# Optimization experiments

Hardware: AMD Instinct MI355X
Metric: run time of the kernel (lower is better)

Reference implementation:

```python
import jax, jax.numpy as jnp
import numpy as np

H = 16
DK = 64
N_PERSIS = 512
D_MODEL = 1024


def setup_inputs() -> dict:
    key = jax.random.key(0)
    ks = jax.random.split(key, 9)
    bs, n, d = 4, 4096, D_MODEL
    inp = {
        "Q": jax.random.normal(ks[0], (bs, n, d), jnp.float32),
        "K": jax.random.normal(ks[1], (bs, n, d), jnp.float32),
        "V": jax.random.normal(ks[2], (bs, n, d), jnp.float32),
        # nn.Linear(d, d, bias=False) weights, applied as x @ W.T
        "WQ": jax.random.normal(ks[3], (d, d), jnp.float32) / np.sqrt(d),
        "WK": jax.random.normal(ks[4], (d, d), jnp.float32) / np.sqrt(d),
        "WV": jax.random.normal(ks[5], (d, d), jnp.float32) / np.sqrt(d),
        "WO": jax.random.normal(ks[6], (d, d), jnp.float32) / np.sqrt(d),
        # persistent memory: MK ~ N(0, 1/dk) * dk**0.5 ; MV ~ N(0, 1/n_persis) * n_persis**0.5
        "MK": jax.random.normal(ks[7], (1, H, N_PERSIS, DK), jnp.float32) * (DK ** 0.5 / DK),
        "MV": jax.random.normal(ks[8], (1, H, N_PERSIS, DK), jnp.float32) * (N_PERSIS ** 0.5 / N_PERSIS),
    }
    return inp


def _split_heads(x, h, dk):
    bs, n, _ = x.shape
    return x.reshape(bs, n, h, dk).transpose(0, 2, 1, 3)  # bs,h,n,dk


def reference(Q, K, V, WQ, WK, WV, WO, MK, MV):
    bs, n, d = Q.shape
    h, dk = MK.shape[1], MK.shape[3]
    q = _split_heads(Q @ WQ.T, h, dk)
    k = _split_heads(K @ WK.T, h, dk)
    v = _split_heads(V @ WV.T, h, dk)
    # concat persistent memory tokens along sequence dim -> m = n + n_persis
    k = jnp.concatenate([k, jnp.broadcast_to(MK, (bs,) + MK.shape[1:])], axis=2)
    v = jnp.concatenate([v, jnp.broadcast_to(MV, (bs,) + MV.shape[1:])], axis=2)
    # dual-softmax linear attention (GDN)
    lamb = jax.nn.softmax(k * dk ** 0.25, axis=2)   # softmax over sequence (m)
    beta = jax.nn.softmax(q, axis=-1)               # softmax over features (dk)
    kv = jnp.einsum('bhmd,bhme->bhde', lamb, v)     # small dk x dk summary
    z = jnp.einsum('bhnd,bhde->bhne', beta, kv)     # bs,h,n,dk
    y = z.transpose(0, 2, 1, 3).reshape(bs, n, h * dk)
    return y @ WO.T
```

## Files before the change

### kernel.cpp

```cpp
#include <hip/hip_runtime.h>
#include <stdint.h>

typedef __attribute__((ext_vector_type(8))) short short8;
typedef __attribute__((ext_vector_type(4))) short short4v;
typedef __attribute__((ext_vector_type(4))) float float4v;
typedef __attribute__((ext_vector_type(4))) unsigned int uint4v;

#define NSEQ   4096
#define DMODEL 1024
#define NHEAD  16
#define DK     64
#define NP     512
#define MTOT   4608
#define NCH    24
#define CH     192
#define SCALE  2.8284271247461903f

__device__ __forceinline__ float b2f(unsigned short u) {
  union { unsigned u; float f; } x; x.u = ((unsigned)u) << 16; return x.f;
}
__device__ __forceinline__ unsigned short f2b(float f) {
  union { float f; unsigned u; } x; x.f = f;
  unsigned r = x.u + 0x7fffu + ((x.u >> 16) & 1u);
  return (unsigned short)(r >> 16);
}
__device__ __forceinline__ void split1(float x, unsigned short& h, unsigned short& l) {
  h = f2b(x);
  l = f2b(x - b2f(h));
}
__device__ __forceinline__ void gload16(const void* g, void* l) {
  __builtin_amdgcn_global_load_lds((const __attribute__((address_space(1))) void*)g,
                                   (__attribute__((address_space(3))) void*)l,
                                   16, 0, 0);
}
__device__ __forceinline__ short8 ld8(const unsigned* p) {
  union { short8 s; short4v h[2]; } u;
  u.h[0] = *(const short4v*)p;
  u.h[1] = *(const short4v*)(p + 2);
  return u.s;
}

__device__ __forceinline__ void swz(int lin, long& brow, long& bcol) {
  brow = (long)(((lin & 7) << 4) | (lin >> 6)) * 128;
  bcol = (long)((lin >> 3) & 7) * 128;
}

__global__ __launch_bounds__(256) void cvt_split(const float* __restrict__ s,
                                                 unsigned short* __restrict__ hi,
                                                 unsigned short* __restrict__ lo, int n) {
  const int i = (blockIdx.x * 256 + threadIdx.x) * 8;
  if (i + 8 > n) return;
  float4v x0 = *(const float4v*)(s + i);
  float4v x1 = *(const float4v*)(s + i + 4);
  unsigned short h[8], l[8];
#pragma unroll
  for (int j = 0; j < 4; ++j) split1(x0[j], h[j], l[j]);
#pragma unroll
  for (int j = 0; j < 4; ++j) split1(x1[j], h[4 + j], l[4 + j]);
  uint4v ph, pl;
#pragma unroll
  for (int j = 0; j < 4; ++j) {
    ph[j] = (unsigned)h[2 * j] | ((unsigned)h[2 * j + 1] << 16);
    pl[j] = (unsigned)l[2 * j] | ((unsigned)l[2 * j + 1] << 16);
  }
  *(uint4v*)(hi + i) = ph;
  *(uint4v*)(lo + i) = pl;
}

__global__ __launch_bounds__(256) void cvt_split4(const float* __restrict__ w0,
                                                  const float* __restrict__ w1,
                                                  const float* __restrict__ w2,
                                                  const float* __restrict__ w3,
                                                  unsigned short* __restrict__ hibase) {
  const int y = blockIdx.y;
  const float* s = (y == 0) ? w0 : (y == 1) ? w1 : (y == 2) ? w2 : w3;
  unsigned short* hi = hibase + (long)y * 2097152;
  unsigned short* lo = hi + 1048576;
  const int i = (blockIdx.x * 256 + threadIdx.x) * 8;
  float4v x0 = *(const float4v*)(s + i);
  float4v x1 = *(const float4v*)(s + i + 4);
  unsigned short h[8], l[8];
#pragma unroll
  for (int j = 0; j < 4; ++j) split1(x0[j], h[j], l[j]);
#pragma unroll
  for (int j = 0; j < 4; ++j) split1(x1[j], h[4 + j], l[4 + j]);
  uint4v ph, pl;
#pragma unroll
  for (int j = 0; j < 4; ++j) {
    ph[j] = (unsigned)h[2 * j] | ((unsigned)h[2 * j + 1] << 16);
    pl[j] = (unsigned)l[2 * j] | ((unsigned)l[2 * j + 1] << 16);
  }
  *(uint4v*)(hi + i) = ph;
  *(uint4v*)(lo + i) = pl;
}

__global__ __launch_bounds__(256) void cvt_hi(const float* __restrict__ s,
                                              unsigned short* __restrict__ hi, int n) {
  const int i = (blockIdx.x * 256 + threadIdx.x) * 8;
  if (i + 8 > n) return;
  float4v x0 = *(const float4v*)(s + i);
  float4v x1 = *(const float4v*)(s + i + 4);
  uint4v ph;
  ph[0] = (unsigned)f2b(x0[0]) | ((unsigned)f2b(x0[1]) << 16);
  ph[1] = (unsigned)f2b(x0[2]) | ((unsigned)f2b(x0[3]) << 16);
  ph[2] = (unsigned)f2b(x1[0]) | ((unsigned)f2b(x1[1]) << 16);
  ph[3] = (unsigned)f2b(x1[2]) | ((unsigned)f2b(x1[3]) << 16);
  *(uint4v*)(hi + i) = ph;
}

template<int BF16OUT>
__global__ __launch_bounds__(256, 4) void gemm_bt(const unsigned short* __restrict__ A,
                                                  const unsigned short* __restrict__ B,
                                                  void* __restrict__ Cv,
                                                  int N, int K) {
  __shared__ unsigned short As[4096];
  __shared__ unsigned short Bs[4096];
  const int tid = threadIdx.x;
  const int w = tid >> 6, lane = tid & 63;
  const int wr = w >> 1, wc = w & 1;
  long brow, bcol; swz(blockIdx.x, brow, bcol);

  const int r0 = tid >> 2;
  const int kc = (tid & 3) * 8;
  const unsigned short* Ag0 = A + (brow + r0) * (long)K + kc;
  const unsigned short* Ag1 = Ag0 + 64L * K;
  const unsigned short* Bg0 = B + (bcol + r0) * (long)K + kc;
  const unsigned short* Bg1 = Bg0 + 64L * K;
  unsigned short* As0 = &As[w * 512];
  unsigned short* Bs0 = &Bs[w * 512];

  float4v acc[4][4];
#pragma unroll
  for (int i = 0; i < 4; ++i)
#pragma unroll
    for (int j = 0; j < 4; ++j) acc[i][j] = (float4v){0.f, 0.f, 0.f, 0.f};

  const int m15 = lane & 15, q8 = (lane >> 4) * 8;

  for (int k0 = 0; k0 < K; k0 += 32) {
    gload16(Ag0 + k0, As0);
    gload16(Ag1 + k0, As0 + 2048);
    gload16(Bg0 + k0, Bs0);
    gload16(Bg1 + k0, Bs0 + 2048);
    __syncthreads();
    short8 af[4], bfr[4];
#pragma unroll
    for (int t = 0; t < 4; ++t) {
      af[t]  = *(const short8*)&As[(wr * 64 + t * 16 + m15) * 32 + q8];
      bfr[t] = *(const short8*)&Bs[(wc * 64 + t * 16 + m15) * 32 + q8];
    }
#pragma unroll
    for (int mt = 0; mt < 4; ++mt)
#pragma unroll
      for (int nt = 0; nt < 4; ++nt)
        acc[mt][nt] = __builtin_amdgcn_mfma_f32_16x16x32_bf16(af[mt], bfr[nt], acc[mt][nt], 0, 0, 0);
    __syncthreads();
  }

  const long col  = bcol + wc * 64 + m15;
  const long rowb = brow + wr * 64 + (lane >> 4) * 4;
  if constexpr (BF16OUT) {
    unsigned short* C = (unsigned short*)Cv;
#pragma unroll
    for (int mt = 0; mt < 4; ++mt)
#pragma unroll
      for (int nt = 0; nt < 4; ++nt)
#pragma unroll
        for (int i = 0; i < 4; ++i)
          C[(rowb + mt * 16 + i) * (long)N + col + nt * 16] = f2b(acc[mt][nt][i]);
  } else {
    float* C = (float*)Cv;
#pragma unroll
    for (int mt = 0; mt < 4; ++mt)
#pragma unroll
      for (int nt = 0; nt < 4; ++nt)
#pragma unroll
        for (int i = 0; i < 4; ++i)
          C[(rowb + mt * 16 + i) * (long)N + col + nt * 16] = acc[mt][nt][i];
  }
}

__global__ __launch_bounds__(256, 4) void gemm_2t(const unsigned short* __restrict__ Ah,
                                                  const unsigned short* __restrict__ Al,
                                                  const unsigned short* __restrict__ Bh,
                                                  float* __restrict__ C,
                                                  int N, int K) {
  __shared__ unsigned short Ash[4096];
  __shared__ unsigned short Asl[4096];
  __shared__ unsigned short Bsh[4096];
  const int tid = threadIdx.x;
  const int w = tid >> 6, lane = tid & 63;
  const int wr = w >> 1, wc = w & 1;
  long brow, bcol; swz(blockIdx.x, brow, bcol);

  const int r0 = tid >> 2;
  const int kc = (tid & 3) * 8;
  const unsigned short* Ahg0 = Ah + (brow + r0) * (long)K + kc;
  const unsigned short* Ahg1 = Ahg0 + 64L * K;
  const unsigned short* Alg0 = Al + (brow + r0) * (long)K + kc;
  const unsigned short* Alg1 = Alg0 + 64L * K;
  const unsigned short* Bhg0 = Bh + (bcol + r0) * (long)K + kc;
  const unsigned short* Bhg1 = Bhg0 + 64L * K;
  unsigned short* Ash0 = &Ash[w * 512];
  unsigned short* Asl0 = &Asl[w * 512];
  unsigned short* Bsh0 = &Bsh[w * 512];

  float4v acc[4][4];
#pragma unroll
  for (int i = 0; i < 4; ++i)
#pragma unroll
    for (int j = 0; j < 4; ++j) acc[i][j] = (float4v){0.f, 0.f, 0.f, 0.f};

  const int m15 = lane & 15, q8 = (lane >> 4) * 8;

  for (int k0 = 0; k0 < K; k0 += 32) {
    gload16(Ahg0 + k0, Ash0);
    gload16(Ahg1 + k0, Ash0 + 2048);
    gload16(Alg0 + k0, Asl0);
    gload16(Alg1 + k0, Asl0 + 2048);
    gload16(Bhg0 + k0, Bsh0);
    gload16(Bhg1 + k0, Bsh0 + 2048);
    __syncthreads();
    short8 ah[4], al[4], bh[4];
#pragma unroll
    for (int t = 0; t < 4; ++t) {
      const int ar = (wr * 64 + t * 16 + m15) * 32 + q8;
      const int br = (wc * 64 + t * 16 + m15) * 32 + q8;
      ah[t] = *(const short8*)&Ash[ar];
      al[t] = *(const short8*)&Asl[ar];
      bh[t] = *(const short8*)&Bsh[br];
    }
#pragma unroll
    for (int mt = 0; mt < 4; ++mt)
#pragma unroll
      for (int nt = 0; nt < 4; ++nt) {
        acc[mt][nt] = __builtin_amdgcn_mfma_f32_16x16x32_bf16(ah[mt], bh[nt], acc[mt][nt], 0, 0, 0);
        acc[mt][nt] = __builtin_amdgcn_mfma_f32_16x16x32_bf16(al[mt], bh[nt], acc[mt][nt], 0, 0, 0);
      }
    __syncthreads();
  }

  const long col  = bcol + wc * 64 + m15;
  const long rowb = brow + wr * 64 + (lane >> 4) * 4;
#pragma unroll
  for (int mt = 0; mt < 4; ++mt)
#pragma unroll
    for (int nt = 0; nt < 4; ++nt)
#pragma unroll
      for (int i = 0; i < 4; ++i)
        C[(rowb + mt * 16 + i) * (long)N + col + nt * 16] = acc[mt][nt][i];
}

__global__ __launch_bounds__(256) void kv_chunk(const float* __restrict__ kf,
                                                const unsigned short* __restrict__ vb,
                                                const float* __restrict__ MK,
                                                const float* __restrict__ MV,
                                                float* __restrict__ pkv,
                                                float* __restrict__ pZ) {
  const int bh = blockIdx.x, c = blockIdx.y;
  const int b = bh >> 4, h = bh & 15;
  const int tid = threadIdx.x;
  const int w = tid >> 6, lane = tid & 63;
  __shared__ unsigned Eh_s[64 * 18];
  __shared__ unsigned El_s[64 * 18];
  __shared__ unsigned Vt_s[64 * 18];

  const int m2  = (tid >> 4) * 2;
  const int d0s = (tid & 15) * 4;

  float4v acc[4];
#pragma unroll
  for (int i = 0; i < 4; ++i) acc[i] = (float4v){0.f, 0.f, 0.f, 0.f};
  float4v zacc = (float4v){0.f, 0.f, 0.f, 0.f};

  short8 ones;
#pragma unroll
  for (int i = 0; i < 8; ++i) ones[i] = (short)0x3F80;

  const int m15 = lane & 15, q8 = (lane >> 4) * 8;
  const int fragoff = m15 * 18 + (q8 >> 1);

  for (int t = 0; t < CH / 32; ++t) {
    const int mt0 = c * CH + t * 32;
    float k0[4], k1[4], v0[4], v1[4];
    if (mt0 < NSEQ) {
      const long base0 = ((long)(b * NSEQ) + mt0 + m2) * DMODEL + h * DK + d0s;
      float4v ka = *(const float4v*)(kf + base0);
      float4v kb = *(const float4v*)(kf + base0 + DMODEL);
      short4v va = *(const short4v*)(vb + base0);
      short4v vc = *(const short4v*)(vb + base0 + DMODEL);
#pragma unroll
      for (int j = 0; j < 4; ++j) {
        k0[j] = ka[j]; k1[j] = kb[j];
        v0[j] = b2f((unsigned short)va[j]); v1[j] = b2f((unsigned short)vc[j]);
      }
    } else {
      const long base0 = ((long)h * NP + (mt0 - NSEQ) + m2) * DK + d0s;
      float4v ka = *(const float4v*)(MK + base0);
      float4v kb = *(const float4v*)(MK + base0 + DK);
      float4v va = *(const float4v*)(MV + base0);
      float4v vc = *(const float4v*)(MV + base0 + DK);
#pragma unroll
      for (int j = 0; j < 4; ++j) { k0[j] = ka[j]; k1[j] = kb[j]; v0[j] = va[j]; v1[j] = vc[j]; }
    }
    __syncthreads();
#pragma unroll
    for (int j = 0; j < 4; ++j) {
      const float e0 = __expf(k0[j] * SCALE);
      const float e1 = __expf(k1[j] * SCALE);
      unsigned short h0, l0, h1, l1;
      split1(e0, h0, l0); split1(e1, h1, l1);
      const int off = (d0s + j) * 18 + (m2 >> 1);
      Eh_s[off] = (unsigned)h0 | ((unsigned)h1 << 16);
      El_s[off] = (unsigned)l0 | ((unsigned)l1 << 16);
      Vt_s[off] = (unsigned)f2b(v0[j]) | ((unsigned)f2b(v1[j]) << 16);
    }
    __syncthreads();
    const short8 a_h = ld8(&Eh_s[w * 16 * 18 + fragoff]);
    const short8 a_l = ld8(&El_s[w * 16 * 18 + fragoff]);
#pragma unroll
    for (int n = 0; n < 4; ++n) {
      const short8 bv = ld8(&Vt_s[n * 16 * 18 + fragoff]);
      acc[n] = __builtin_amdgcn_mfma_f32_16x16x32_bf16(a_h, bv, acc[n], 0, 0, 0);
      acc[n] = __builtin_amdgcn_mfma_f32_16x16x32_bf16(a_l, bv, acc[n], 0, 0, 0);
    }
    zacc = __builtin_amdgcn_mfma_f32_16x16x32_bf16(a_h, ones, zacc, 0, 0, 0);
    zacc = __builtin_amdgcn_mfma_f32_16x16x32_bf16(a_l, ones, zacc, 0, 0, 0);
  }

  const int row = (lane >> 4) * 4;
  float* pk = pkv + (((long)(bh * NCH + c)) << 12);
#pragma unroll
  for (int n = 0; n < 4; ++n)
#pragma unroll
    for (int i = 0; i < 4; ++i)
      pk[(w * 16 + row + i) * 64 + n * 16 + m15] = acc[n][i];
  if (m15 == 0) {
#pragma unroll
    for (int i = 0; i < 4; ++i)
      pZ[(bh * NCH + c) * 64 + w * 16 + row + i] = zacc[i];
  }
}

__global__ __launch_bounds__(256) void reduce_kv2(const float* __restrict__ pkv,
                                                  const float* __restrict__ pZ,
                                                  float* __restrict__ kvT) {
  const int idx = blockIdx.x * 256 + threadIdx.x;
  const int bh = idx >> 12, de = idx & 4095, d = de >> 6, e = de & 63;
  float s = 0.f;
#pragma unroll
  for (int c = 0; c < NCH; ++c) s += pkv[(((long)(bh * NCH + c)) << 12) + de];
  float Z = 0.f;
#pragma unroll
  for (int c = 0; c < NCH; ++c) Z += pZ[(bh * NCH + c) * 64 + d];
  kvT[((long)bh << 12) + e * 64 + d] = s / Z;
}

__global__ __launch_bounds__(256) void beta_z(const unsigned short* __restrict__ qb,
                                              const float* __restrict__ kvT,
                                              unsigned short* __restrict__ y) {
  const int bh = blockIdx.y, b = bh >> 4, h = bh & 15;
  const int t0 = blockIdx.x * 256;
  const int tid = threadIdx.x;
  const int w = tid >> 6, lane = tid & 63;
  __shared__ unsigned short beta_s[256 * 72];
  __shared__ unsigned short kvh_s[64 * 72], kvl_s[64 * 72];

  {
    const unsigned short* qp = qb + ((long)(b * NSEQ) + t0 + tid) * DMODEL + h * DK;
    float vals[64];
#pragma unroll
    for (int i = 0; i < 8; ++i) {
      const short8 r = *(const short8*)(qp + i * 8);
#pragma unroll
      for (int j = 0; j < 8; ++j) vals[i * 8 + j] = b2f((unsigned short)r[j]);
    }
    float mx = vals[0];
#pragma unroll
    for (int i = 1; i < 64; ++i) mx = fmaxf(mx, vals[i]);
    float sum = 0.f;
#pragma unroll
    for (int i = 0; i < 64; ++i) { vals[i] = __expf(vals[i] - mx); sum += vals[i]; }
    const float inv = 1.f / sum;
#pragma unroll
    for (int i = 0; i < 64; ++i) beta_s[tid * 72 + i] = f2b(vals[i] * inv);
  }
  for (int c = tid; c < 4096; c += 256) {
    const float v = kvT[((long)bh << 12) + c];
    const int e = c >> 6, d = c & 63;
    unsigned short hh, ll;
    split1(v, hh, ll);
    kvh_s[e * 72 + d] = hh;
    kvl_s[e * 72 + d] = ll;
  }
  __syncthreads();

  float4v acc[4][4];
#pragma unroll
  for (int i = 0; i < 4; ++i)
#pragma unroll
    for (int j = 0; j < 4; ++j) acc[i][j] = (float4v){0.f, 0.f, 0.f, 0.f};
  const int m15 = lane & 15, q8 = (lane >> 4) * 8;
#pragma unroll
  for (int k0 = 0; k0 < 64; k0 += 32) {
    short8 af[4], bh_[4], bl_[4];
#pragma unroll
    for (int t = 0; t < 4; ++t) {
      af[t]  = *(const short8*)&beta_s[(w * 64 + t * 16 + m15) * 72 + k0 + q8];
      bh_[t] = *(const short8*)&kvh_s[(t * 16 + m15) * 72 + k0 + q8];
      bl_[t] = *(const short8*)&kvl_s[(t * 16 + m15) * 72 + k0 + q8];
    }
#pragma unroll
    for (int mt = 0; mt < 4; ++mt)
#pragma unroll
      for (int nt = 0; nt < 4; ++nt) {
        acc[mt][nt] = __builtin_amdgcn_mfma_f32_16x16x32_bf16(af[mt], bh_[nt], acc[mt][nt], 0, 0, 0);
        acc[mt][nt] = __builtin_amdgcn_mfma_f32_16x16x32_bf16(af[mt], bl_[nt], acc[mt][nt], 0, 0, 0);
      }
  }
  const long ybase = ((long)b * NSEQ) * DMODEL + (long)h * DK;
  const int q4 = (lane >> 4) * 4;
#pragma unroll
  for (int mt = 0; mt < 4; ++mt)
#pragma unroll
    for (int nt = 0; nt < 4; ++nt)
#pragma unroll
      for (int i = 0; i < 4; ++i) {
        const int t = t0 + w * 64 + mt * 16 + q4 + i;
        y[ybase + (long)t * DMODEL + nt * 16 + m15] = f2b(acc[mt][nt][i]);
      }
}

extern "C" void kernel_launch(void* const* d_in, const int* in_sizes, int n_in,
                              void* d_out, int out_size, void* d_ws, size_t ws_size,
                              hipStream_t stream) {
  const float* Q  = (const float*)d_in[0];
  const float* Kk = (const float*)d_in[1];
  const float* V  = (const float*)d_in[2];
  const float* WQ = (const float*)d_in[3];
  const float* WK = (const float*)d_in[4];
  const float* WV = (const float*)d_in[5];
  const float* WO = (const float*)d_in[6];
  const float* MK = (const float*)d_in[7];
  const float* MV = (const float*)d_in[8];

  char* ws = (char*)d_ws;
  unsigned short* R1 = (unsigned short*)(ws);
  unsigned short* R2 = (unsigned short*)(ws + 33554432);
  float*          kf = (float*)(ws + 67108864);
  const long WB = 134217728;
  unsigned short* Wbase = (unsigned short*)(ws + WB);
  unsigned short* WQh = Wbase;
  unsigned short* WKh = (unsigned short*)(ws + WB + 4194304);
  unsigned short* WVh = (unsigned short*)(ws + WB + 8388608);
  unsigned short* WOh = (unsigned short*)(ws + WB + 12582912);
  const long S = 150994944;
  float* pZ  = (float*)(ws + S);
  float* kvT = (float*)(ws + S + 8683520);
  float* pkv = (float*)R1;

  const dim3 blk(256);
  const int N = 1024, K = 1024;
  const int NELEM = 4 * NSEQ * DMODEL;

  cvt_split4<<<dim3(512, 4), blk, 0, stream>>>(WQ, WK, WV, WO, Wbase);

  cvt_split<<<8192, blk, 0, stream>>>(Kk, R1, R2, NELEM);
  gemm_2t<<<1024, blk, 0, stream>>>(R1, R2, WKh, kf, N, K);

  cvt_hi<<<8192, blk, 0, stream>>>(V, R1, NELEM);
  gemm_bt<1><<<1024, blk, 0, stream>>>(R1, WVh, (void*)R2, N, K);

  kv_chunk<<<dim3(64, NCH), blk, 0, stream>>>(kf, R2, MK, MV, pkv, pZ);
  reduce_kv2<<<1024, blk, 0, stream>>>(pkv, pZ, kvT);

  cvt_hi<<<8192, blk, 0, stream>>>(Q, R1, NELEM);
  gemm_bt<1><<<1024, blk, 0, stream>>>(R1, WQh, (void*)R2, N, K);

  beta_z<<<dim3(16, 64), blk, 0, stream>>>(R2, kvT, R1);

  gemm_bt<0><<<1024, blk, 0, stream>>>(R1, WOh, (float*)d_out, N, K);
}
```

Measured before the change: 478.4 us.

## Fuse exp/split into K-projection GEMM and fuse Q GEMM with beta softmax

The K-projection GEMM epilogue now applies exp(k*scale) and writes hi/lo bf16 halves, so kv_chunk loads bf16 pairs instead of fp32 keys and skips the exp. The Q-projection GEMM is fused with the feature softmax and the beta·kv product: the 128x128 tile covers two whole heads, the softmax uses row shuffles, and the z result is written directly. This removes the separate beta_z kernel and the round trip of q through memory. In exchange, the fused kernel keeps a larger shared pool at lower occupancy and reads kvT from global memory per block.

```diff
diff --git a/kernel.cpp b/kernel.cpp
--- a/kernel.cpp
+++ b/kernel.cpp
@@ -180,11 +180,12 @@
   }
 }
 
-__global__ __launch_bounds__(256, 4) void gemm_2t(const unsigned short* __restrict__ Ah,
-                                                  const unsigned short* __restrict__ Al,
-                                                  const unsigned short* __restrict__ Bh,
-                                                  float* __restrict__ C,
-                                                  int N, int K) {
+__global__ __launch_bounds__(256, 4) void gemm_2t_exp(const unsigned short* __restrict__ Ah,
+                                                      const unsigned short* __restrict__ Al,
+                                                      const unsigned short* __restrict__ Bh,
+                                                      unsigned short* __restrict__ Eh,
+                                                      unsigned short* __restrict__ El,
+                                                      int N, int K) {
   __shared__ unsigned short Ash[4096];
   __shared__ unsigned short Asl[4096];
   __shared__ unsigned short Bsh[4096];
@@ -247,11 +248,18 @@
 #pragma unroll
     for (int nt = 0; nt < 4; ++nt)
 #pragma unroll
-      for (int i = 0; i < 4; ++i)
-        C[(rowb + mt * 16 + i) * (long)N + col + nt * 16] = acc[mt][nt][i];
-}
-
-__global__ __launch_bounds__(256) void kv_chunk(const float* __restrict__ kf,
+      for (int i = 0; i < 4; ++i) {
+        const float e = __expf(acc[mt][nt][i] * SCALE);
+        unsigned short hh, ll;
+        split1(e, hh, ll);
+        const long idx = (rowb + mt * 16 + i) * (long)N + col + nt * 16;
+        Eh[idx] = hh;
+        El[idx] = ll;
+      }
+}
+
+__global__ __launch_bounds__(256) void kv_chunk(const unsigned short* __restrict__ Ehg,
+                                                const unsigned short* __restrict__ Elg,
                                                 const unsigned short* __restrict__ vb,
                                                 const float* __restrict__ MK,
                                                 const float* __restrict__ MV,
@@ -282,17 +290,20 @@
 
   for (int t = 0; t < CH / 32; ++t) {
     const int mt0 = c * CH + t * 32;
-    float k0[4], k1[4], v0[4], v1[4];
+    unsigned short eh0[4], eh1[4], el0[4], el1[4], vv0[4], vv1[4];
     if (mt0 < NSEQ) {
       const long base0 = ((long)(b * NSEQ) + mt0 + m2) * DMODEL + h * DK + d0s;
-      float4v ka = *(const float4v*)(kf + base0);
-      float4v kb = *(const float4v*)(kf + base0 + DMODEL);
-      short4v va = *(const short4v*)(vb + base0);
-      short4v vc = *(const short4v*)(vb + base0 + DMODEL);
+      short4v a0 = *(const short4v*)(Ehg + base0);
+      short4v a1 = *(const short4v*)(Ehg + base0 + DMODEL);
+      short4v b0 = *(const short4v*)(Elg + base0);
+      short4v b1 = *(const short4v*)(Elg + base0 + DMODEL);
+      short4v c0 = *(const short4v*)(vb + base0);
+      short4v c1 = *(const short4v*)(vb + base0 + DMODEL);
 #pragma unroll
       for (int j = 0; j < 4; ++j) {
-        k0[j] = ka[j]; k1[j] = kb[j];
-        v0[j] = b2f((unsigned short)va[j]); v1[j] = b2f((unsigned short)vc[j]);
+        eh0[j] = (unsigned short)a0[j]; eh1[j] = (unsigned short)a1[j];
+        el0[j] = (unsigned short)b0[j]; el1[j] = (unsigned short)b1[j];
+        vv0[j] = (unsigned short)c0[j]; vv1[j] = (unsigned short)c1[j];
       }
     } else {
       const long base0 = ((long)h * NP + (mt0 - NSEQ) + m2) * DK + d0s;
@@ -301,19 +312,19 @@
       float4v va = *(const float4v*)(MV + base0);
       float4v vc = *(const float4v*)(MV + base0 + DK);
 #pragma unroll
-      for (int j = 0; j < 4; ++j) { k0[j] = ka[j]; k1[j] = kb[j]; v0[j] = va[j]; v1[j] = vc[j]; }
+      for (int j = 0; j < 4; ++j) {
+        split1(__expf(ka[j] * SCALE), eh0[j], el0[j]);
+        split1(__expf(kb[j] * SCALE), eh1[j], el1[j]);
+        vv0[j] = f2b(va[j]); vv1[j] = f2b(vc[j]);
+      }
     }
     __syncthreads();
 #pragma unroll
     for (int j = 0; j < 4; ++j) {
-      const float e0 = __expf(k0[j] * SCALE);
-      const float e1 = __expf(k1[j] * SCALE);
-      unsigned short h0, l0, h1, l1;
-      split1(e0, h0, l0); split1(e1, h1, l1);
       const int off = (d0s + j) * 18 + (m2 >> 1);
-      Eh_s[off] = (unsigned)h0 | ((unsigned)h1 << 16);
-      El_s[off] = (unsigned)l0 | ((unsigned)l1 << 16);
-      Vt_s[off] = (unsigned)f2b(v0[j]) | ((unsigned)f2b(v1[j]) << 16);
+      Eh_s[off] = (unsigned)eh0[j] | ((unsigned)eh1[j] << 16);
+      El_s[off] = (unsigned)el0[j] | ((unsigned)el1[j] << 16);
+      Vt_s[off] = (unsigned)vv0[j] | ((unsigned)vv1[j] << 16);
     }
     __syncthreads();
     const short8 a_h = ld8(&Eh_s[w * 16 * 18 + fragoff]);
@@ -356,79 +367,123 @@
   kvT[((long)bh << 12) + e * 64 + d] = s / Z;
 }
 
-__global__ __launch_bounds__(256) void beta_z(const unsigned short* __restrict__ qb,
-                                              const float* __restrict__ kvT,
-                                              unsigned short* __restrict__ y) {
-  const int bh = blockIdx.y, b = bh >> 4, h = bh & 15;
-  const int t0 = blockIdx.x * 256;
+__global__ __launch_bounds__(256, 2) void gemm_q_beta(const unsigned short* __restrict__ A,
+                                                      const unsigned short* __restrict__ B,
+                                                      const float* __restrict__ kvT,
+                                                      unsigned short* __restrict__ y) {
+  __shared__ unsigned short pool[17408];
+  unsigned short* As = pool;
+  unsigned short* Bs = pool + 4096;
+  unsigned short* beta_s = pool;
+
   const int tid = threadIdx.x;
   const int w = tid >> 6, lane = tid & 63;
-  __shared__ unsigned short beta_s[256 * 72];
-  __shared__ unsigned short kvh_s[64 * 72], kvl_s[64 * 72];
-
-  {
-    const unsigned short* qp = qb + ((long)(b * NSEQ) + t0 + tid) * DMODEL + h * DK;
-    float vals[64];
-#pragma unroll
-    for (int i = 0; i < 8; ++i) {
-      const short8 r = *(const short8*)(qp + i * 8);
-#pragma unroll
-      for (int j = 0; j < 8; ++j) vals[i * 8 + j] = b2f((unsigned short)r[j]);
-    }
-    float mx = vals[0];
-#pragma unroll
-    for (int i = 1; i < 64; ++i) mx = fmaxf(mx, vals[i]);
-    float sum = 0.f;
-#pragma unroll
-    for (int i = 0; i < 64; ++i) { vals[i] = __expf(vals[i] - mx); sum += vals[i]; }
-    const float inv = 1.f / sum;
-#pragma unroll
-    for (int i = 0; i < 64; ++i) beta_s[tid * 72 + i] = f2b(vals[i] * inv);
-  }
-  for (int c = tid; c < 4096; c += 256) {
-    const float v = kvT[((long)bh << 12) + c];
-    const int e = c >> 6, d = c & 63;
-    unsigned short hh, ll;
-    split1(v, hh, ll);
-    kvh_s[e * 72 + d] = hh;
-    kvl_s[e * 72 + d] = ll;
+  const int wr = w >> 1, wc = w & 1;
+  long brow, bcol; swz(blockIdx.x, brow, bcol);
+  const int K = 1024;
+
+  const int r0 = tid >> 2;
+  const int kc = (tid & 3) * 8;
+  const unsigned short* Ag0 = A + (brow + r0) * (long)K + kc;
+  const unsigned short* Ag1 = Ag0 + 64L * K;
+  const unsigned short* Bg0 = B + (bcol + r0) * (long)K + kc;
+  const unsigned short* Bg1 = Bg0 + 64L * K;
+  unsigned short* As0 = &As[w * 512];
+  unsigned short* Bs0 = &Bs[w * 512];
+
+  float4v acc[4][4];
+#pragma unroll
+  for (int i = 0; i < 4; ++i)
+#pragma unroll
+    for (int j = 0; j < 4; ++j) acc[i][j] = (float4v){0.f, 0.f, 0.f, 0.f};
+
+  const int m15 = lane & 15, q8 = (lane >> 4) * 8, q4 = (lane >> 4) * 4;
+
+  for (int k0 = 0; k0 < K; k0 += 32) {
+    gload16(Ag0 + k0, As0);
+    gload16(Ag1 + k0, As0 + 2048);
+    gload16(Bg0 + k0, Bs0);
+    gload16(Bg1 + k0, Bs0 + 2048);
+    __syncthreads();
+    short8 af[4], bfr[4];
+#pragma unroll
+    for (int t = 0; t < 4; ++t) {
+      af[t]  = *(const short8*)&As[(wr * 64 + t * 16 + m15) * 32 + q8];
+      bfr[t] = *(const short8*)&Bs[(wc * 64 + t * 16 + m15) * 32 + q8];
+    }
+#pragma unroll
+    for (int mt = 0; mt < 4; ++mt)
+#pragma unroll
+      for (int nt = 0; nt < 4; ++nt)
+        acc[mt][nt] = __builtin_amdgcn_mfma_f32_16x16x32_bf16(af[mt], bfr[nt], acc[mt][nt], 0, 0, 0);
+    __syncthreads();
+  }
+
+#pragma unroll
+  for (int mt = 0; mt < 4; ++mt) {
+#pragma unroll
+    for (int i = 0; i < 4; ++i) {
+      float mx = fmaxf(fmaxf(acc[mt][0][i], acc[mt][1][i]),
+                       fmaxf(acc[mt][2][i], acc[mt][3][i]));
+#pragma unroll
+      for (int s = 1; s < 16; s <<= 1) mx = fmaxf(mx, __shfl_xor(mx, s));
+      float e[4], sum = 0.f;
+#pragma unroll
+      for (int nt = 0; nt < 4; ++nt) { e[nt] = __expf(acc[mt][nt][i] - mx); sum += e[nt]; }
+#pragma unroll
+      for (int s = 1; s < 16; s <<= 1) sum += __shfl_xor(sum, s);
+      const float inv = 1.f / sum;
+      const int r = wr * 64 + mt * 16 + q4 + i;
+#pragma unroll
+      for (int nt = 0; nt < 4; ++nt)
+        beta_s[r * 136 + wc * 64 + nt * 16 + m15] = f2b(e[nt] * inv);
+    }
   }
   __syncthreads();
 
-  float4v acc[4][4];
+  const int hb = (int)(bcol >> 6) + wc;
+  const int bb = (int)(brow >> 12);
+  const long kvbase = ((long)(bb * 16 + hb)) << 12;
+
+  float4v zacc[4][4];
 #pragma unroll
   for (int i = 0; i < 4; ++i)
 #pragma unroll
-    for (int j = 0; j < 4; ++j) acc[i][j] = (float4v){0.f, 0.f, 0.f, 0.f};
-  const int m15 = lane & 15, q8 = (lane >> 4) * 8;
-#pragma unroll
-  for (int k0 = 0; k0 < 64; k0 += 32) {
-    short8 af[4], bh_[4], bl_[4];
-#pragma unroll
-    for (int t = 0; t < 4; ++t) {
-      af[t]  = *(const short8*)&beta_s[(w * 64 + t * 16 + m15) * 72 + k0 + q8];
-      bh_[t] = *(const short8*)&kvh_s[(t * 16 + m15) * 72 + k0 + q8];
-      bl_[t] = *(const short8*)&kvl_s[(t * 16 + m15) * 72 + k0 + q8];
-    }
-#pragma unroll
-    for (int mt = 0; mt < 4; ++mt)
-#pragma unroll
-      for (int nt = 0; nt < 4; ++nt) {
-        acc[mt][nt] = __builtin_amdgcn_mfma_f32_16x16x32_bf16(af[mt], bh_[nt], acc[mt][nt], 0, 0, 0);
-        acc[mt][nt] = __builtin_amdgcn_mfma_f32_16x16x32_bf16(af[mt], bl_[nt], acc[mt][nt], 0, 0, 0);
+    for (int j = 0; j < 4; ++j) zacc[i][j] = (float4v){0.f, 0.f, 0.f, 0.f};
+
+#pragma unroll
+  for (int nt = 0; nt < 4; ++nt) {
+    short8 bh2[2], bl2[2];
+#pragma unroll
+    for (int kk = 0; kk < 2; ++kk) {
+      const float* kp = kvT + kvbase + (nt * 16 + m15) * 64 + kk * 32 + q8;
+      float4v k0v = *(const float4v*)kp;
+      float4v k1v = *(const float4v*)(kp + 4);
+      unsigned short hh[8], ll[8];
+#pragma unroll
+      for (int j = 0; j < 4; ++j) { split1(k0v[j], hh[j], ll[j]); split1(k1v[j], hh[4 + j], ll[4 + j]); }
+#pragma unroll
+      for (int j = 0; j < 8; ++j) { bh2[kk][j] = (short)hh[j]; bl2[kk][j] = (short)ll[j]; }
+    }
+#pragma unroll
+    for (int mt = 0; mt < 4; ++mt) {
+#pragma unroll
+      for (int kk = 0; kk < 2; ++kk) {
+        const short8 af = *(const short8*)&beta_s[(wr * 64 + mt * 16 + m15) * 136 + wc * 64 + kk * 32 + q8];
+        zacc[mt][nt] = __builtin_amdgcn_mfma_f32_16x16x32_bf16(af, bh2[kk], zacc[mt][nt], 0, 0, 0);
+        zacc[mt][nt] = __builtin_amdgcn_mfma_f32_16x16x32_bf16(af, bl2[kk], zacc[mt][nt], 0, 0, 0);
       }
-  }
-  const long ybase = ((long)b * NSEQ) * DMODEL + (long)h * DK;
-  const int q4 = (lane >> 4) * 4;
+    }
+  }
+
 #pragma unroll
   for (int mt = 0; mt < 4; ++mt)
 #pragma unroll
     for (int nt = 0; nt < 4; ++nt)
 #pragma unroll
-      for (int i = 0; i < 4; ++i) {
-        const int t = t0 + w * 64 + mt * 16 + q4 + i;
-        y[ybase + (long)t * DMODEL + nt * 16 + m15] = f2b(acc[mt][nt][i]);
-      }
+      for (int i = 0; i < 4; ++i)
+        y[(brow + wr * 64 + mt * 16 + q4 + i) * (long)DMODEL + hb * 64 + nt * 16 + m15] =
+            f2b(zacc[mt][nt][i]);
 }
 
 extern "C" void kernel_launch(void* const* d_in, const int* in_sizes, int n_in,
@@ -447,7 +502,8 @@
   char* ws = (char*)d_ws;
   unsigned short* R1 = (unsigned short*)(ws);
   unsigned short* R2 = (unsigned short*)(ws + 33554432);
-  float*          kf = (float*)(ws + 67108864);
+  unsigned short* Eh = (unsigned short*)(ws + 67108864);
+  unsigned short* El = (unsigned short*)(ws + 100663296);
   const long WB = 134217728;
   unsigned short* Wbase = (unsigned short*)(ws + WB);
   unsigned short* WQh = Wbase;
@@ -466,18 +522,16 @@
   cvt_split4<<<dim3(512, 4), blk, 0, stream>>>(WQ, WK, WV, WO, Wbase);
 
   cvt_split<<<8192, blk, 0, stream>>>(Kk, R1, R2, NELEM);
-  gemm_2t<<<1024, blk, 0, stream>>>(R1, R2, WKh, kf, N, K);
+  gemm_2t_exp<<<1024, blk, 0, stream>>>(R1, R2, WKh, Eh, El, N, K);
 
   cvt_hi<<<8192, blk, 0, stream>>>(V, R1, NELEM);
   gemm_bt<1><<<1024, blk, 0, stream>>>(R1, WVh, (void*)R2, N, K);
 
-  kv_chunk<<<dim3(64, NCH), blk, 0, stream>>>(kf, R2, MK, MV, pkv, pZ);
+  kv_chunk<<<dim3(64, NCH), blk, 0, stream>>>(Eh, El, R2, MK, MV, pkv, pZ);
   reduce_kv2<<<1024, blk, 0, stream>>>(pkv, pZ, kvT);
 
   cvt_hi<<<8192, blk, 0, stream>>>(Q, R1, NELEM);
-  gemm_bt<1><<<1024, blk, 0, stream>>>(R1, WQh, (void*)R2, N, K);
-
-  beta_z<<<dim3(16, 64), blk, 0, stream>>>(R2, kvT, R1);
-
-  gemm_bt<0><<<1024, blk, 0, stream>>>(R1, WOh, (float*)d_out, N, K);
-}
+  gemm_q_beta<<<1024, blk, 0, stream>>>(R1, WQh, kvT, R2);
+
+  gemm_bt<0><<<1024, blk, 0, stream>>>(R2, WOh, (float*)d_out, N, K);
+}
```

Result: no change. 482.5 us (+0.9%).
